# Optimization experiments

Measured on AMD Instinct MI355X. Metric: run time of the kernel, lower is better.

## Reference

```python
import jax, jax.numpy as jnp
import numpy as np

BANDWIDTHS = (1.0, 2.0, 3.0)


def setup_inputs() -> dict:
    key = jax.random.key(0)
    kx, ky = jax.random.split(key)
    x = jax.random.normal(kx, (8192, 512), dtype=jnp.float32)
    y = jax.random.normal(ky, (8192, 512), dtype=jnp.float32)
    return {"x": x, "y": y}


def _multi_bw_kernel_mean(a, b):
    # pairwise squared distances: [n, m]
    a_norm = jnp.sum(a * a, axis=1)[:, None]
    b_norm = jnp.sum(b * b, axis=1)[None, :]
    dxy = a_norm + b_norm - 2.0 * (a @ b.T)
    k = sum(jnp.exp(-0.5 * dxy / bw) for bw in BANDWIDTHS)
    return jnp.mean(k)


def reference(x, y):
    return (_multi_bw_kernel_mean(x, x)
            + _multi_bw_kernel_mean(y, y)
            - 2.0 * _multi_bw_kernel_mean(x, y))
```

## Files before the change

### kernel.cpp

```cpp
#include <hip/hip_runtime.h>

#define NR  8192
#define DIM 512
#define BM  256
#define BK  64
#define NT  8

typedef __attribute__((ext_vector_type(8))) short bf16x8;
typedef __attribute__((ext_vector_type(4))) float f32x4;
typedef unsigned short u16;
typedef unsigned int   u32;

__device__ __forceinline__ void gload16(const void* g, void* l) {
    __builtin_amdgcn_global_load_lds((const __attribute__((address_space(1))) void*)g,
                                     (__attribute__((address_space(3))) void*)l,
                                     16, 0, 0);
}

__global__ __launch_bounds__(256) void conv_bf16(const float* __restrict__ x,
                                                 const float* __restrict__ y,
                                                 u16* __restrict__ xb, u16* __restrict__ yb,
                                                 float* __restrict__ xn, float* __restrict__ yn) {
    int gw = (blockIdx.x * 256 + threadIdx.x) >> 6;
    int lane = threadIdx.x & 63;
    if (gw >= 2 * NR) return;
    int row = (gw < NR) ? gw : gw - NR;
    const float* src = (gw < NR) ? x : y;
    u16*   dst = (gw < NR) ? xb : yb;
    float* nrm = (gw < NR) ? xn : yn;

    const float4* p = (const float4*)(src + (size_t)row * DIM);
    float4 v0 = p[lane * 2], v1 = p[lane * 2 + 1];
    float vv[8] = {v0.x, v0.y, v0.z, v0.w, v1.x, v1.y, v1.z, v1.w};
    u16 us[8]; float s = 0.f;
    #pragma unroll
    for (int i = 0; i < 8; ++i) {
        u32 u = __float_as_uint(vv[i]);
        u16 b = (u16)((u + 0x7FFFu + ((u >> 16) & 1u)) >> 16);
        us[i] = b;
        float bf = __uint_as_float(((u32)b) << 16);
        s += bf * bf;
    }
    *(bf16x8*)(dst + (size_t)row * DIM + lane * 8) = *(const bf16x8*)us;
    #pragma unroll
    for (int off = 32; off; off >>= 1) s += __shfl_down(s, off, 64);
    if (lane == 0) nrm[row] = s;
}

__global__ void zero_kernel(double* acc) {
    if (threadIdx.x == 0 && blockIdx.x == 0) *acc = 0.0;
}

__global__ void finalize_kernel(const double* __restrict__ acc, float* __restrict__ out) {
    if (threadIdx.x == 0 && blockIdx.x == 0) {
        double n2 = (double)NR * (double)NR;
        out[0] = (float)(*acc / n2);
    }
}

__global__ __launch_bounds__(512, 2) void mmd_bf16(const u16* __restrict__ xb, const u16* __restrict__ yb,
                                                   const float* __restrict__ xn, const float* __restrict__ yn,
                                                   double* __restrict__ acc) {
    int f = (blockIdx.x & 7) * 260 + (blockIdx.x >> 3);
    int z, bi, bj;
    if (f < 1056) {
        z = (f < 528) ? 0 : 1;
        int t = (f < 528) ? f : f - 528;
        int r = (int)((sqrtf(8.f * t + 1.f) - 1.f) * 0.5f);
        while ((r + 1) * (r + 2) / 2 <= t) ++r;
        while (r * (r + 1) / 2 > t) --r;
        bi = t - r * (r + 1) / 2;
        bj = r;
    } else {
        z = 2; int t = f - 1056; bi = t >> 5; bj = t & 31;
    }
    const u16*   A  = (z == 1) ? yb : xb;
    const u16*   B  = (z == 0) ? xb : yb;
    const float* an = (z == 1) ? yn : xn;
    const float* bn = (z == 0) ? xn : yn;
    const float wgt = (z == 2) ? -2.f : ((bi == bj) ? 1.f : 2.f);
    const int bm = bi * BM, bnc = bj * BM;

    __shared__ __align__(16) u16 Al[2][BM * BK];
    __shared__ __align__(16) u16 Bl[2][BM * BK];

    const int tid = threadIdx.x, w = tid >> 6, lane = tid & 63;
    const int wm = w >> 2, wn = w & 3;
    const int srow = lane >> 3;
    const int dslot = (lane & 7) ^ srow;
    const int fr = lane & 15, kg = lane >> 4;

    int raO[8], rbO[4];
    #pragma unroll
    for (int fm = 0; fm < 8; ++fm) raO[fm] = (wm * 128 + fm * 16 + fr) * BK;
    #pragma unroll
    for (int fn = 0; fn < 4; ++fn) rbO[fn] = (wn * 64 + fn * 16 + fr) * BK;
    const int s0 = ((kg)     ^ (lane & 7)) * 8;
    const int s1 = ((4 + kg) ^ (lane & 7)) * 8;

    f32x4 acc4[8][4];
    #pragma unroll
    for (int i = 0; i < 8; ++i)
        #pragma unroll
        for (int j = 0; j < 4; ++j)
            acc4[i][j] = {0.f, 0.f, 0.f, 0.f};

    const size_t aRow = (size_t)(bm  + w * 32 + srow) * DIM + dslot * 8;
    const size_t bRow = (size_t)(bnc + w * 32 + srow) * DIM + dslot * 8;

#define STAGE(kt, buf)                                                              \
    {                                                                               \
        _Pragma("unroll")                                                           \
        for (int q = 0; q < 4; ++q) {                                               \
            const int rb_ = w * 32 + q * 8;                                         \
            gload16(A + aRow + (size_t)q * 8 * DIM + (kt) * BK, &Al[buf][rb_ * BK]);\
            gload16(B + bRow + (size_t)q * 8 * DIM + (kt) * BK, &Bl[buf][rb_ * BK]);\
        }                                                                           \
    }

    STAGE(0, 0)
    STAGE(1, 1)
    asm volatile("s_waitcnt vmcnt(8)" ::: "memory");
    __builtin_amdgcn_s_barrier();

    #pragma unroll
    for (int kt = 0; kt < NT; ++kt) {
        const int cur = kt & 1;
        const u16* Ab = &Al[cur][0];
        const u16* Bb = &Bl[cur][0];

        {
            bf16x8 af[8], bf[4];
            #pragma unroll
            for (int fm = 0; fm < 8; ++fm) af[fm] = *(const bf16x8*)(Ab + raO[fm] + s0);
            #pragma unroll
            for (int fn = 0; fn < 4; ++fn) bf[fn] = *(const bf16x8*)(Bb + rbO[fn] + s0);
            __builtin_amdgcn_s_setprio(1);
            #pragma unroll
            for (int fm = 0; fm < 8; ++fm)
                #pragma unroll
                for (int fn = 0; fn < 4; ++fn)
                    acc4[fm][fn] = __builtin_amdgcn_mfma_f32_16x16x32_bf16(af[fm], bf[fn], acc4[fm][fn], 0, 0, 0);
            __builtin_amdgcn_s_setprio(0);
        }
        {
            bf16x8 af[8], bf[4];
            #pragma unroll
            for (int fm = 0; fm < 8; ++fm) af[fm] = *(const bf16x8*)(Ab + raO[fm] + s1);
            #pragma unroll
            for (int fn = 0; fn < 4; ++fn) bf[fn] = *(const bf16x8*)(Bb + rbO[fn] + s1);
            __builtin_amdgcn_s_setprio(1);
            #pragma unroll
            for (int fm = 0; fm < 8; ++fm)
                #pragma unroll
                for (int fn = 0; fn < 4; ++fn)
                    acc4[fm][fn] = __builtin_amdgcn_mfma_f32_16x16x32_bf16(af[fm], bf[fn], acc4[fm][fn], 0, 0, 0);
            __builtin_amdgcn_s_setprio(0);
        }

        if (kt + 1 < NT) {
            asm volatile("s_waitcnt lgkmcnt(0)" ::: "memory");
            __builtin_amdgcn_s_barrier();
            if (kt + 2 < NT) {
                STAGE(kt + 2, cur)
                asm volatile("s_waitcnt vmcnt(8)" ::: "memory");
            } else {
                asm volatile("s_waitcnt vmcnt(0)" ::: "memory");
            }
            __builtin_amdgcn_s_barrier();
        }
    }

    float lsum = 0.f;
    #pragma unroll
    for (int fm = 0; fm < 8; ++fm) {
        const f32x4 anv = *(const f32x4*)(an + bm + wm * 128 + fm * 16 + kg * 4);
        #pragma unroll
        for (int fn = 0; fn < 4; ++fn) {
            const float bnv = bn[bnc + wn * 64 + fn * 16 + fr];
            #pragma unroll
            for (int j = 0; j < 4; ++j) {
                float d  = anv[j] + bnv - 2.0f * acc4[fm][fn][j];
                float t  = __expf(d * (-1.0f / 12.0f));
                float t2 = t * t, t3 = t2 * t;
                lsum += t2 + t3 + t3 * t3;
            }
        }
    }
    #pragma unroll
    for (int off = 32; off; off >>= 1) lsum += __shfl_down(lsum, off, 64);

    float* wsum = (float*)&Al[0][0];
    if (lane == 0) wsum[w] = lsum;
    __syncthreads();
    if (tid == 0) {
        float bs = 0.f;
        #pragma unroll
        for (int i = 0; i < 8; ++i) bs += wsum[i];
        atomicAdd(acc, (double)(bs * wgt));
    }
#undef STAGE
}

extern "C" void kernel_launch(void* const* d_in, const int* in_sizes, int n_in,
                              void* d_out, int out_size, void* d_ws, size_t ws_size,
                              hipStream_t stream) {
    const float* x = (const float*)d_in[0];
    const float* y = (const float*)d_in[1];
    float* out = (float*)d_out;
    char* ws = (char*)d_ws;

    const size_t bBytes = (size_t)NR * DIM * 2;
    u16*   xb = (u16*)ws;
    u16*   yb = (u16*)(ws + bBytes);
    float* xn = (float*)(ws + 2 * bBytes);
    float* yn = (float*)(ws + 2 * bBytes + (size_t)NR * 4);
    double* acc = (double*)(ws + 2 * bBytes + 2 * (size_t)NR * 4);

    zero_kernel<<<1, 64, 0, stream>>>(acc);
    conv_bf16<<<(2 * NR) / 4, 256, 0, stream>>>(x, y, xb, yb, xn, yn);
    mmd_bf16<<<2080, 512, 0, stream>>>(xb, yb, xn, yn, acc);
    finalize_kernel<<<1, 64, 0, stream>>>(acc, out);
}
```

Measured before the change: 195.2 us.

## Switch GEMM main loop to 4-stage K32 pipeline with interleaved A/B staging

Replaces the double-buffered BK=64 K-loop with a four-slot ring of K=32 slices, prefetching three slices ahead. A and B loads for the next slice are issued in separate halves of each iteration, between two half-tile MFMA groups separated by barriers. The LDS swizzle is also redone for the 32-wide rows. The goal is to hide global-load latency better and spread LDS reads across the MFMA work. The cost is more barriers per K step and the same LDS footprint. The vmcnt accounting is delicate and could race if it is off.

Result: slower. 219.3 us (+12.4%).

```diff
diff --git a/kernel.cpp b/kernel.cpp
--- a/kernel.cpp
+++ b/kernel.cpp
@@ -3,8 +3,8 @@
 #define NR  8192
 #define DIM 512
 #define BM  256
-#define BK  64
-#define NT  8
+#define KS  32
+#define NKS 16
 
 typedef __attribute__((ext_vector_type(8))) short bf16x8;
 typedef __attribute__((ext_vector_type(4))) float f32x4;
@@ -81,22 +81,23 @@
     const float wgt = (z == 2) ? -2.f : ((bi == bj) ? 1.f : 2.f);
     const int bm = bi * BM, bnc = bj * BM;
 
-    __shared__ __align__(16) u16 Al[2][BM * BK];
-    __shared__ __align__(16) u16 Bl[2][BM * BK];
+    __shared__ __align__(16) u16 Al[4][BM * KS];
+    __shared__ __align__(16) u16 Bl[4][BM * KS];
 
     const int tid = threadIdx.x, w = tid >> 6, lane = tid & 63;
     const int wm = w >> 2, wn = w & 3;
-    const int srow = lane >> 3;
-    const int dslot = (lane & 7) ^ srow;
     const int fr = lane & 15, kg = lane >> 4;
 
+    const int srow  = lane >> 2;
+    const int sslot = (lane & 3) ^ ((lane >> 4) & 3);
+
+    const int sw   = (fr >> 2) & 3;
+    const int aoff = (kg ^ sw) * 8;
     int raO[8], rbO[4];
     #pragma unroll
-    for (int fm = 0; fm < 8; ++fm) raO[fm] = (wm * 128 + fm * 16 + fr) * BK;
-    #pragma unroll
-    for (int fn = 0; fn < 4; ++fn) rbO[fn] = (wn * 64 + fn * 16 + fr) * BK;
-    const int s0 = ((kg)     ^ (lane & 7)) * 8;
-    const int s1 = ((4 + kg) ^ (lane & 7)) * 8;
+    for (int fm = 0; fm < 8; ++fm) raO[fm] = (wm * 128 + fm * 16 + fr) * KS + aoff;
+    #pragma unroll
+    for (int fn = 0; fn < 4; ++fn) rbO[fn] = (wn * 64 + fn * 16 + fr) * KS + aoff;
 
     f32x4 acc4[8][4];
     #pragma unroll
@@ -105,71 +106,69 @@
         for (int j = 0; j < 4; ++j)
             acc4[i][j] = {0.f, 0.f, 0.f, 0.f};
 
-    const size_t aRow = (size_t)(bm  + w * 32 + srow) * DIM + dslot * 8;
-    const size_t bRow = (size_t)(bnc + w * 32 + srow) * DIM + dslot * 8;
-
-#define STAGE(kt, buf)                                                              \
-    {                                                                               \
-        _Pragma("unroll")                                                           \
-        for (int q = 0; q < 4; ++q) {                                               \
-            const int rb_ = w * 32 + q * 8;                                         \
-            gload16(A + aRow + (size_t)q * 8 * DIM + (kt) * BK, &Al[buf][rb_ * BK]);\
-            gload16(B + bRow + (size_t)q * 8 * DIM + (kt) * BK, &Bl[buf][rb_ * BK]);\
-        }                                                                           \
-    }
-
-    STAGE(0, 0)
-    STAGE(1, 1)
+    const size_t aBase = (size_t)(bm  + w * 32 + srow) * DIM + sslot * 8;
+    const size_t bBase = (size_t)(bnc + w * 32 + srow) * DIM + sslot * 8;
+
+#define STAGEA(kt, slot)                                                                   \
+    {                                                                                      \
+        gload16(A + aBase +            (size_t)(kt) * KS, &Al[slot][(w * 32     ) * KS]);  \
+        gload16(A + aBase + 16 * DIM + (size_t)(kt) * KS, &Al[slot][(w * 32 + 16) * KS]);  \
+    }
+#define STAGEB(kt, slot)                                                                   \
+    {                                                                                      \
+        gload16(B + bBase +            (size_t)(kt) * KS, &Bl[slot][(w * 32     ) * KS]);  \
+        gload16(B + bBase + 16 * DIM + (size_t)(kt) * KS, &Bl[slot][(w * 32 + 16) * KS]);  \
+    }
+
+    STAGEA(0, 0) STAGEB(0, 0)
+    STAGEA(1, 1) STAGEB(1, 1)
+    STAGEA(2, 2) STAGEB(2, 2)
     asm volatile("s_waitcnt vmcnt(8)" ::: "memory");
     __builtin_amdgcn_s_barrier();
 
     #pragma unroll
-    for (int kt = 0; kt < NT; ++kt) {
-        const int cur = kt & 1;
-        const u16* Ab = &Al[cur][0];
-        const u16* Bb = &Bl[cur][0];
-
-        {
-            bf16x8 af[8], bf[4];
+    for (int kt = 0; kt < NKS; ++kt) {
+        const int cs = kt & 3;
+        const int ns = (kt + 3) & 3;
+        const u16* Ab = &Al[cs][0];
+        const u16* Bb = &Bl[cs][0];
+
+        if (kt <= NKS - 4) STAGEA(kt + 3, ns)
+        bf16x8 bfr[4], af0[4];
+        #pragma unroll
+        for (int fn = 0; fn < 4; ++fn) bfr[fn] = *(const bf16x8*)(Bb + rbO[fn]);
+        #pragma unroll
+        for (int fm = 0; fm < 4; ++fm) af0[fm] = *(const bf16x8*)(Ab + raO[fm]);
+        __builtin_amdgcn_s_barrier();
+        __builtin_amdgcn_s_setprio(1);
+        #pragma unroll
+        for (int fm = 0; fm < 4; ++fm)
             #pragma unroll
-            for (int fm = 0; fm < 8; ++fm) af[fm] = *(const bf16x8*)(Ab + raO[fm] + s0);
+            for (int fn = 0; fn < 4; ++fn)
+                acc4[fm][fn] = __builtin_amdgcn_mfma_f32_16x16x32_bf16(af0[fm], bfr[fn], acc4[fm][fn], 0, 0, 0);
+        __builtin_amdgcn_s_setprio(0);
+        __builtin_amdgcn_s_barrier();
+
+        if (kt <= NKS - 4) STAGEB(kt + 3, ns)
+        bf16x8 af1[4];
+        #pragma unroll
+        for (int fm = 0; fm < 4; ++fm) af1[fm] = *(const bf16x8*)(Ab + raO[fm + 4]);
+        __builtin_amdgcn_s_barrier();
+        __builtin_amdgcn_s_setprio(1);
+        #pragma unroll
+        for (int fm = 0; fm < 4; ++fm)
             #pragma unroll
-            for (int fn = 0; fn < 4; ++fn) bf[fn] = *(const bf16x8*)(Bb + rbO[fn] + s0);
-            __builtin_amdgcn_s_setprio(1);
-            #pragma unroll
-            for (int fm = 0; fm < 8; ++fm)
-                #pragma unroll
-                for (int fn = 0; fn < 4; ++fn)
-                    acc4[fm][fn] = __builtin_amdgcn_mfma_f32_16x16x32_bf16(af[fm], bf[fn], acc4[fm][fn], 0, 0, 0);
-            __builtin_amdgcn_s_setprio(0);
-        }
-        {
-            bf16x8 af[8], bf[4];
-            #pragma unroll
-            for (int fm = 0; fm < 8; ++fm) af[fm] = *(const bf16x8*)(Ab + raO[fm] + s1);
-            #pragma unroll
-            for (int fn = 0; fn < 4; ++fn) bf[fn] = *(const bf16x8*)(Bb + rbO[fn] + s1);
-            __builtin_amdgcn_s_setprio(1);
-            #pragma unroll
-            for (int fm = 0; fm < 8; ++fm)
-                #pragma unroll
-                for (int fn = 0; fn < 4; ++fn)
-                    acc4[fm][fn] = __builtin_amdgcn_mfma_f32_16x16x32_bf16(af[fm], bf[fn], acc4[fm][fn], 0, 0, 0);
-            __builtin_amdgcn_s_setprio(0);
-        }
-
-        if (kt + 1 < NT) {
-            asm volatile("s_waitcnt lgkmcnt(0)" ::: "memory");
-            __builtin_amdgcn_s_barrier();
-            if (kt + 2 < NT) {
-                STAGE(kt + 2, cur)
-                asm volatile("s_waitcnt vmcnt(8)" ::: "memory");
-            } else {
-                asm volatile("s_waitcnt vmcnt(0)" ::: "memory");
-            }
-            __builtin_amdgcn_s_barrier();
-        }
-    }
+            for (int fn = 0; fn < 4; ++fn)
+                acc4[fm + 4][fn] = __builtin_amdgcn_mfma_f32_16x16x32_bf16(af1[fm], bfr[fn], acc4[fm + 4][fn], 0, 0, 0);
+        __builtin_amdgcn_s_setprio(0);
+
+        if (kt <= NKS - 4)      { asm volatile("s_waitcnt vmcnt(8)" ::: "memory"); }
+        else if (kt == NKS - 3) { asm volatile("s_waitcnt vmcnt(4)" ::: "memory"); }
+        else if (kt == NKS - 2) { asm volatile("s_waitcnt vmcnt(0)" ::: "memory"); }
+        if (kt < NKS - 1) __builtin_amdgcn_s_barrier();
+    }
+#undef STAGEA
+#undef STAGEB
 
     float lsum = 0.f;
     #pragma unroll
@@ -199,7 +198,6 @@
         for (int i = 0; i < 8; ++i) bs += wsum[i];
         atomicAdd(acc, (double)(bs * wgt));
     }
-#undef STAGE
 }
 
 extern "C" void kernel_launch(void* const* d_in, const int* in_sizes, int n_in,
```

## Split MFMA k-step into four barrier-separated quadrant phases with interleaved LDS loads

Applied to the files above, without the earlier changes.

Restructures the inner k-loop into four phases, each computing one 4x2 quadrant of the accumulator tile over the full BK=64. LDS fragment loads for the next quadrant are issued between phases, and the global-to-LDS prefetch moves into the last phase. Each phase is entered through barriers and s_setprio so waves alternate between memory and MFMA work, ping-pong style. This is meant to overlap LDS reads and prefetch with matrix math and lower register pressure, at the cost of extra workgroup barriers per k-step.

Measured after the change: 207.6 us. 6.4% more time.

```diff
diff --git a/kernel.cpp b/kernel.cpp
--- a/kernel.cpp
+++ b/kernel.cpp
@@ -3,7 +3,6 @@
 #define NR  8192
 #define DIM 512
 #define BM  256
-#define BK  64
 #define NT  8
 
 typedef __attribute__((ext_vector_type(8))) short bf16x8;
@@ -81,8 +80,8 @@
     const float wgt = (z == 2) ? -2.f : ((bi == bj) ? 1.f : 2.f);
     const int bm = bi * BM, bnc = bj * BM;
 
-    __shared__ __align__(16) u16 Al[2][BM * BK];
-    __shared__ __align__(16) u16 Bl[2][BM * BK];
+    __shared__ __align__(16) u16 Al[2][BM * 64];
+    __shared__ __align__(16) u16 Bl[2][BM * 64];
 
     const int tid = threadIdx.x, w = tid >> 6, lane = tid & 63;
     const int wm = w >> 2, wn = w & 3;
@@ -92,9 +91,9 @@
 
     int raO[8], rbO[4];
     #pragma unroll
-    for (int fm = 0; fm < 8; ++fm) raO[fm] = (wm * 128 + fm * 16 + fr) * BK;
-    #pragma unroll
-    for (int fn = 0; fn < 4; ++fn) rbO[fn] = (wn * 64 + fn * 16 + fr) * BK;
+    for (int fm = 0; fm < 8; ++fm) raO[fm] = (wm * 128 + fm * 16 + fr) * 64;
+    #pragma unroll
+    for (int fn = 0; fn < 4; ++fn) rbO[fn] = (wn * 64 + fn * 16 + fr) * 64;
     const int s0 = ((kg)     ^ (lane & 7)) * 8;
     const int s1 = ((4 + kg) ^ (lane & 7)) * 8;
 
@@ -113,10 +112,30 @@
         _Pragma("unroll")                                                           \
         for (int q = 0; q < 4; ++q) {                                               \
             const int rb_ = w * 32 + q * 8;                                         \
-            gload16(A + aRow + (size_t)q * 8 * DIM + (kt) * BK, &Al[buf][rb_ * BK]);\
-            gload16(B + bRow + (size_t)q * 8 * DIM + (kt) * BK, &Bl[buf][rb_ * BK]);\
+            gload16(A + aRow + (size_t)q * 8 * DIM + (kt) * 64, &Al[buf][rb_ * 64]);\
+            gload16(B + bRow + (size_t)q * 8 * DIM + (kt) * 64, &Bl[buf][rb_ * 64]);\
         }                                                                           \
     }
+
+#define LDA(fm_, so_) (*(const bf16x8*)(Ab + raO[fm_] + (so_)))
+#define LDB(fn_, so_) (*(const bf16x8*)(Bb + rbO[fn_] + (so_)))
+
+#define PH_ENTER                                                    \
+    __builtin_amdgcn_s_barrier();                                   \
+    asm volatile("s_waitcnt lgkmcnt(0)" ::: "memory");              \
+    __builtin_amdgcn_sched_barrier(0);                              \
+    __builtin_amdgcn_s_setprio(1);
+
+#define MFMAQ(MH, NH, BF)                                                           \
+    _Pragma("unroll")                                                               \
+    for (int fp = 0; fp < 4; ++fp)                                                  \
+        _Pragma("unroll")                                                           \
+        for (int fq = 0; fq < 2; ++fq) {                                            \
+            acc4[(MH)*4+fp][(NH)*2+fq] = __builtin_amdgcn_mfma_f32_16x16x32_bf16(   \
+                af[fp][0], BF[fq][0], acc4[(MH)*4+fp][(NH)*2+fq], 0, 0, 0);         \
+            acc4[(MH)*4+fp][(NH)*2+fq] = __builtin_amdgcn_mfma_f32_16x16x32_bf16(   \
+                af[fp][1], BF[fq][1], acc4[(MH)*4+fp][(NH)*2+fq], 0, 0, 0);         \
+        }
 
     STAGE(0, 0)
     STAGE(1, 1)
@@ -128,41 +147,38 @@
         const int cur = kt & 1;
         const u16* Ab = &Al[cur][0];
         const u16* Bb = &Bl[cur][0];
-
-        {
-            bf16x8 af[8], bf[4];
-            #pragma unroll
-            for (int fm = 0; fm < 8; ++fm) af[fm] = *(const bf16x8*)(Ab + raO[fm] + s0);
-            #pragma unroll
-            for (int fn = 0; fn < 4; ++fn) bf[fn] = *(const bf16x8*)(Bb + rbO[fn] + s0);
-            __builtin_amdgcn_s_setprio(1);
-            #pragma unroll
-            for (int fm = 0; fm < 8; ++fm)
-                #pragma unroll
-                for (int fn = 0; fn < 4; ++fn)
-                    acc4[fm][fn] = __builtin_amdgcn_mfma_f32_16x16x32_bf16(af[fm], bf[fn], acc4[fm][fn], 0, 0, 0);
-            __builtin_amdgcn_s_setprio(0);
-        }
-        {
-            bf16x8 af[8], bf[4];
-            #pragma unroll
-            for (int fm = 0; fm < 8; ++fm) af[fm] = *(const bf16x8*)(Ab + raO[fm] + s1);
-            #pragma unroll
-            for (int fn = 0; fn < 4; ++fn) bf[fn] = *(const bf16x8*)(Bb + rbO[fn] + s1);
-            __builtin_amdgcn_s_setprio(1);
-            #pragma unroll
-            for (int fm = 0; fm < 8; ++fm)
-                #pragma unroll
-                for (int fn = 0; fn < 4; ++fn)
-                    acc4[fm][fn] = __builtin_amdgcn_mfma_f32_16x16x32_bf16(af[fm], bf[fn], acc4[fm][fn], 0, 0, 0);
-            __builtin_amdgcn_s_setprio(0);
-        }
+        bf16x8 af[4][2], bf0[2][2], bf1[2][2];
+
+        #pragma unroll
+        for (int i = 0; i < 4; ++i) { af[i][0] = LDA(i, s0); af[i][1] = LDA(i, s1); }
+        #pragma unroll
+        for (int j = 0; j < 2; ++j) { bf0[j][0] = LDB(j, s0); bf0[j][1] = LDB(j, s1); }
+        PH_ENTER
+        MFMAQ(0, 0, bf0)
+        __builtin_amdgcn_s_setprio(0);
+        __builtin_amdgcn_s_barrier();
+
+        #pragma unroll
+        for (int j = 0; j < 2; ++j) { bf1[j][0] = LDB(2 + j, s0); bf1[j][1] = LDB(2 + j, s1); }
+        PH_ENTER
+        MFMAQ(0, 1, bf1)
+        __builtin_amdgcn_s_setprio(0);
+        __builtin_amdgcn_s_barrier();
+
+        #pragma unroll
+        for (int i = 0; i < 4; ++i) { af[i][0] = LDA(4 + i, s0); af[i][1] = LDA(4 + i, s1); }
+        PH_ENTER
+        MFMAQ(1, 1, bf1)
+        __builtin_amdgcn_s_setprio(0);
+        __builtin_amdgcn_s_barrier();
+
+        if (kt + 2 < NT) STAGE(kt + 2, cur)
+        PH_ENTER
+        MFMAQ(1, 0, bf0)
+        __builtin_amdgcn_s_setprio(0);
 
         if (kt + 1 < NT) {
-            asm volatile("s_waitcnt lgkmcnt(0)" ::: "memory");
-            __builtin_amdgcn_s_barrier();
-            if (kt + 2 < NT) {
-                STAGE(kt + 2, cur)
+            if (kt < NT - 2) {
                 asm volatile("s_waitcnt vmcnt(8)" ::: "memory");
             } else {
                 asm volatile("s_waitcnt vmcnt(0)" ::: "memory");
@@ -170,6 +186,11 @@
             __builtin_amdgcn_s_barrier();
         }
     }
+#undef STAGE
+#undef LDA
+#undef LDB
+#undef PH_ENTER
+#undef MFMAQ
 
     float lsum = 0.f;
     #pragma unroll
@@ -199,7 +220,6 @@
         for (int i = 0; i < 8; ++i) bs += wsum[i];
         atomicAdd(acc, (double)(bs * wgt));
     }
-#undef STAGE
 }
 
 extern "C" void kernel_launch(void* const* d_in, const int* in_sizes, int n_in,
```

## Make MMD kernel persistent with cross-tile prefetch of next tile's operands

Applied to the files above, without the earlier changes.

Replaces the 2080-block grid with 256 persistent blocks, each processing a contiguous range of about 8 tiles. The first two K-stages of the next tile are prefetched while the current tile finishes and its exp epilogue runs, hiding load latency and removing per-block launch and tail costs. Occupancy drops from 2 to 1 block per CU, s_setprio hints are removed, and the static partition of 2080 tiles over 256 blocks may leave some load imbalance.

Result: slower. 202.4 us (+3.7%).

```diff
diff --git a/kernel.cpp b/kernel.cpp
--- a/kernel.cpp
+++ b/kernel.cpp
@@ -3,7 +3,6 @@
 #define NR  8192
 #define DIM 512
 #define BM  256
-#define BK  64
 #define NT  8
 
 typedef __attribute__((ext_vector_type(8))) short bf16x8;
@@ -58,11 +57,7 @@
     }
 }
 
-__global__ __launch_bounds__(512, 2) void mmd_bf16(const u16* __restrict__ xb, const u16* __restrict__ yb,
-                                                   const float* __restrict__ xn, const float* __restrict__ yn,
-                                                   double* __restrict__ acc) {
-    int f = (blockIdx.x & 7) * 260 + (blockIdx.x >> 3);
-    int z, bi, bj;
+__device__ __forceinline__ void tri_decode(int f, int& z, int& bi, int& bj) {
     if (f < 1056) {
         z = (f < 528) ? 0 : 1;
         int t = (f < 528) ? f : f - 528;
@@ -74,15 +69,19 @@
     } else {
         z = 2; int t = f - 1056; bi = t >> 5; bj = t & 31;
     }
-    const u16*   A  = (z == 1) ? yb : xb;
-    const u16*   B  = (z == 0) ? xb : yb;
-    const float* an = (z == 1) ? yn : xn;
-    const float* bn = (z == 0) ? xn : yn;
-    const float wgt = (z == 2) ? -2.f : ((bi == bj) ? 1.f : 2.f);
-    const int bm = bi * BM, bnc = bj * BM;
-
-    __shared__ __align__(16) u16 Al[2][BM * BK];
-    __shared__ __align__(16) u16 Bl[2][BM * BK];
+}
+
+__global__ __launch_bounds__(512, 1) void mmd_bf16(const u16* __restrict__ xb, const u16* __restrict__ yb,
+                                                   const float* __restrict__ xn, const float* __restrict__ yn,
+                                                   double* __restrict__ acc) {
+    __shared__ __align__(16) u16 Al[2][BM * 64];
+    __shared__ __align__(16) u16 Bl[2][BM * 64];
+    __shared__ float wsum[8];
+
+    const int p  = blockIdx.x;
+    const int pp = (p & 7) * 32 + (p >> 3);
+    const int f0 = (pp * 65) >> 3;
+    const int f1 = ((pp + 1) * 65) >> 3;
 
     const int tid = threadIdx.x, w = tid >> 6, lane = tid & 63;
     const int wm = w >> 2, wn = w & 3;
@@ -92,114 +91,135 @@
 
     int raO[8], rbO[4];
     #pragma unroll
-    for (int fm = 0; fm < 8; ++fm) raO[fm] = (wm * 128 + fm * 16 + fr) * BK;
-    #pragma unroll
-    for (int fn = 0; fn < 4; ++fn) rbO[fn] = (wn * 64 + fn * 16 + fr) * BK;
+    for (int fm = 0; fm < 8; ++fm) raO[fm] = (wm * 128 + fm * 16 + fr) * 64;
+    #pragma unroll
+    for (int fn = 0; fn < 4; ++fn) rbO[fn] = (wn * 64 + fn * 16 + fr) * 64;
     const int s0 = ((kg)     ^ (lane & 7)) * 8;
     const int s1 = ((4 + kg) ^ (lane & 7)) * 8;
 
-    f32x4 acc4[8][4];
-    #pragma unroll
-    for (int i = 0; i < 8; ++i)
-        #pragma unroll
-        for (int j = 0; j < 4; ++j)
-            acc4[i][j] = {0.f, 0.f, 0.f, 0.f};
-
-    const size_t aRow = (size_t)(bm  + w * 32 + srow) * DIM + dslot * 8;
-    const size_t bRow = (size_t)(bnc + w * 32 + srow) * DIM + dslot * 8;
-
-#define STAGE(kt, buf)                                                              \
+#define STAGE1(P_, RB_, KT_, DST_)                                                  \
     {                                                                               \
         _Pragma("unroll")                                                           \
         for (int q = 0; q < 4; ++q) {                                               \
             const int rb_ = w * 32 + q * 8;                                         \
-            gload16(A + aRow + (size_t)q * 8 * DIM + (kt) * BK, &Al[buf][rb_ * BK]);\
-            gload16(B + bRow + (size_t)q * 8 * DIM + (kt) * BK, &Bl[buf][rb_ * BK]);\
+            gload16(P_ + RB_ + (size_t)q * 8 * DIM + (KT_) * 64, &DST_[rb_ * 64]);  \
         }                                                                           \
     }
 
-    STAGE(0, 0)
-    STAGE(1, 1)
-    asm volatile("s_waitcnt vmcnt(8)" ::: "memory");
-    __builtin_amdgcn_s_barrier();
-
-    #pragma unroll
-    for (int kt = 0; kt < NT; ++kt) {
-        const int cur = kt & 1;
-        const u16* Ab = &Al[cur][0];
-        const u16* Bb = &Bl[cur][0];
-
-        {
-            bf16x8 af[8], bf[4];
-            #pragma unroll
-            for (int fm = 0; fm < 8; ++fm) af[fm] = *(const bf16x8*)(Ab + raO[fm] + s0);
-            #pragma unroll
-            for (int fn = 0; fn < 4; ++fn) bf[fn] = *(const bf16x8*)(Bb + rbO[fn] + s0);
-            __builtin_amdgcn_s_setprio(1);
-            #pragma unroll
-            for (int fm = 0; fm < 8; ++fm)
-                #pragma unroll
-                for (int fn = 0; fn < 4; ++fn)
-                    acc4[fm][fn] = __builtin_amdgcn_mfma_f32_16x16x32_bf16(af[fm], bf[fn], acc4[fm][fn], 0, 0, 0);
-            __builtin_amdgcn_s_setprio(0);
-        }
-        {
-            bf16x8 af[8], bf[4];
-            #pragma unroll
-            for (int fm = 0; fm < 8; ++fm) af[fm] = *(const bf16x8*)(Ab + raO[fm] + s1);
-            #pragma unroll
-            for (int fn = 0; fn < 4; ++fn) bf[fn] = *(const bf16x8*)(Bb + rbO[fn] + s1);
-            __builtin_amdgcn_s_setprio(1);
-            #pragma unroll
-            for (int fm = 0; fm < 8; ++fm)
-                #pragma unroll
-                for (int fn = 0; fn < 4; ++fn)
-                    acc4[fm][fn] = __builtin_amdgcn_mfma_f32_16x16x32_bf16(af[fm], bf[fn], acc4[fm][fn], 0, 0, 0);
-            __builtin_amdgcn_s_setprio(0);
-        }
-
-        if (kt + 1 < NT) {
-            asm volatile("s_waitcnt lgkmcnt(0)" ::: "memory");
-            __builtin_amdgcn_s_barrier();
-            if (kt + 2 < NT) {
-                STAGE(kt + 2, cur)
-                asm volatile("s_waitcnt vmcnt(8)" ::: "memory");
-            } else {
-                asm volatile("s_waitcnt vmcnt(0)" ::: "memory");
+    int z, bi, bj; tri_decode(f0, z, bi, bj);
+    const u16*   A  = (z == 1) ? yb : xb;
+    const u16*   B  = (z == 0) ? xb : yb;
+    const float* an = (z == 1) ? yn : xn;
+    const float* bn = (z == 0) ? xn : yn;
+    float wgt = (z == 2) ? -2.f : ((bi == bj) ? 1.f : 2.f);
+    int bm = bi * BM, bnc = bj * BM;
+    size_t aRow = (size_t)(bm  + w * 32 + srow) * DIM + dslot * 8;
+    size_t bRow = (size_t)(bnc + w * 32 + srow) * DIM + dslot * 8;
+
+    STAGE1(A, aRow, 0, Al[0]) STAGE1(B, bRow, 0, Bl[0])
+    STAGE1(A, aRow, 1, Al[1]) STAGE1(B, bRow, 1, Bl[1])
+
+    for (int f = f0; f < f1; ++f) {
+        const bool hasNext = (f + 1 < f1);
+        const u16 *nA = A, *nB = B; const float *nan_ = an, *nbn_ = bn;
+        float nwgt = wgt; int nbm = bm, nbnc = bnc; size_t naRow = aRow, nbRow = bRow;
+        if (hasNext) {
+            int z2, bi2, bj2; tri_decode(f + 1, z2, bi2, bj2);
+            nA  = (z2 == 1) ? yb : xb;
+            nB  = (z2 == 0) ? xb : yb;
+            nan_ = (z2 == 1) ? yn : xn;
+            nbn_ = (z2 == 0) ? xn : yn;
+            nwgt = (z2 == 2) ? -2.f : ((bi2 == bj2) ? 1.f : 2.f);
+            nbm = bi2 * BM; nbnc = bj2 * BM;
+            naRow = (size_t)(nbm  + w * 32 + srow) * DIM + dslot * 8;
+            nbRow = (size_t)(nbnc + w * 32 + srow) * DIM + dslot * 8;
+        }
+
+        asm volatile("s_waitcnt vmcnt(8)" ::: "memory");
+        __builtin_amdgcn_s_barrier();
+
+        f32x4 acc4[8][4];
+        #pragma unroll
+        for (int i = 0; i < 8; ++i)
+            #pragma unroll
+            for (int j = 0; j < 4; ++j)
+                acc4[i][j] = {0.f, 0.f, 0.f, 0.f};
+
+        #pragma unroll
+        for (int kt = 0; kt < NT; ++kt) {
+            const int cur = kt & 1;
+            const u16* Ab = &Al[cur][0];
+            const u16* Bb = &Bl[cur][0];
+
+            #pragma unroll
+            for (int ph = 0; ph < 2; ++ph) {
+                const int so = ph ? s1 : s0;
+                bf16x8 af[8], bfr[4];
+                #pragma unroll
+                for (int fm = 0; fm < 8; ++fm) af[fm] = *(const bf16x8*)(Ab + raO[fm] + so);
+                #pragma unroll
+                for (int fn = 0; fn < 4; ++fn) bfr[fn] = *(const bf16x8*)(Bb + rbO[fn] + so);
+                #pragma unroll
+                for (int fm = 0; fm < 8; ++fm)
+                    #pragma unroll
+                    for (int fn = 0; fn < 4; ++fn)
+                        acc4[fm][fn] = __builtin_amdgcn_mfma_f32_16x16x32_bf16(af[fm], bfr[fn], acc4[fm][fn], 0, 0, 0);
             }
-            __builtin_amdgcn_s_barrier();
-        }
-    }
-
-    float lsum = 0.f;
-    #pragma unroll
-    for (int fm = 0; fm < 8; ++fm) {
-        const f32x4 anv = *(const f32x4*)(an + bm + wm * 128 + fm * 16 + kg * 4);
-        #pragma unroll
-        for (int fn = 0; fn < 4; ++fn) {
-            const float bnv = bn[bnc + wn * 64 + fn * 16 + fr];
-            #pragma unroll
-            for (int j = 0; j < 4; ++j) {
-                float d  = anv[j] + bnv - 2.0f * acc4[fm][fn][j];
-                float t  = __expf(d * (-1.0f / 12.0f));
-                float t2 = t * t, t3 = t2 * t;
-                lsum += t2 + t3 + t3 * t3;
+
+            if (kt + 1 < NT) {
+                asm volatile("s_waitcnt lgkmcnt(0)" ::: "memory");
+                __builtin_amdgcn_s_barrier();
+                if (kt + 2 < NT) {
+                    STAGE1(A, aRow, kt + 2, Al[cur]) STAGE1(B, bRow, kt + 2, Bl[cur])
+                    asm volatile("s_waitcnt vmcnt(8)" ::: "memory");
+                } else {
+                    if (hasNext) {
+                        STAGE1(nA, naRow, 0, Al[0]) STAGE1(nB, nbRow, 0, Bl[0])
+                        asm volatile("s_waitcnt vmcnt(8)" ::: "memory");
+                    } else {
+                        asm volatile("s_waitcnt vmcnt(0)" ::: "memory");
+                    }
+                }
+                __builtin_amdgcn_s_barrier();
             }
         }
-    }
-    #pragma unroll
-    for (int off = 32; off; off >>= 1) lsum += __shfl_down(lsum, off, 64);
-
-    float* wsum = (float*)&Al[0][0];
-    if (lane == 0) wsum[w] = lsum;
-    __syncthreads();
-    if (tid == 0) {
-        float bs = 0.f;
-        #pragma unroll
-        for (int i = 0; i < 8; ++i) bs += wsum[i];
-        atomicAdd(acc, (double)(bs * wgt));
-    }
-#undef STAGE
+
+        asm volatile("s_waitcnt lgkmcnt(0)" ::: "memory");
+        __builtin_amdgcn_s_barrier();
+        if (hasNext) { STAGE1(nA, nbRow - nbRow + naRow, 1, Al[1]) STAGE1(nB, nbRow, 1, Bl[1]) }
+
+        float lsum = 0.f;
+        #pragma unroll
+        for (int fm = 0; fm < 8; ++fm) {
+            const f32x4 anv = *(const f32x4*)(an + bm + wm * 128 + fm * 16 + kg * 4);
+            #pragma unroll
+            for (int fn = 0; fn < 4; ++fn) {
+                const float bnv = bn[bnc + wn * 64 + fn * 16 + fr];
+                #pragma unroll
+                for (int j = 0; j < 4; ++j) {
+                    float d  = anv[j] + bnv - 2.0f * acc4[fm][fn][j];
+                    float t  = __expf(d * (-1.0f / 12.0f));
+                    float t2 = t * t, t3 = t2 * t;
+                    lsum += t2 + t3 + t3 * t3;
+                }
+            }
+        }
+        #pragma unroll
+        for (int off = 32; off; off >>= 1) lsum += __shfl_down(lsum, off, 64);
+        if (lane == 0) wsum[w] = lsum;
+        asm volatile("s_waitcnt lgkmcnt(0)" ::: "memory");
+        __builtin_amdgcn_s_barrier();
+        if (tid == 0) {
+            float bs = 0.f;
+            #pragma unroll
+            for (int i = 0; i < 8; ++i) bs += wsum[i];
+            atomicAdd(acc, (double)(bs * wgt));
+        }
+
+        A = nA; B = nB; an = nan_; bn = nbn_; wgt = nwgt;
+        bm = nbm; bnc = nbnc; aRow = naRow; bRow = nbRow;
+    }
+#undef STAGE1
 }
 
 extern "C" void kernel_launch(void* const* d_in, const int* in_sizes, int n_in,
@@ -219,6 +239,6 @@
 
     zero_kernel<<<1, 64, 0, stream>>>(acc);
     conv_bf16<<<(2 * NR) / 4, 256, 0, stream>>>(x, y, xb, yb, xn, yn);
-    mmd_bf16<<<2080, 512, 0, stream>>>(xb, yb, xn, yn, acc);
+    mmd_bf16<<<256, 512, 0, stream>>>(xb, yb, xn, yn, acc);
     finalize_kernel<<<1, 64, 0, stream>>>(acc, out);
 }
```
